# Kernel optimization log

Measured on AMD Instinct MI355X. Metric: run time of the kernel, lower is better.

The kernel has to match this reference:

```python
import jax, jax.numpy as jnp
import numpy as np

B, NS, NF, D, H = 64, 16, 4096, 128, 256  # batch, n_slots, n_feat, slot_dim, mlp_hidden
EPS_LN = 1e-5
EPS_ATT = 1e-8


def _layernorm(x, g, b):
    mu = x.mean(-1, keepdims=True)
    var = x.var(-1, keepdims=True)
    return (x - mu) / jnp.sqrt(var + EPS_LN) * g + b


def setup_inputs() -> dict:
    key = jax.random.key(0)
    ks = jax.random.split(key, 8)
    s = 0.02  # init scale for weights
    return {
        "t": jnp.zeros((), jnp.float32),
        "slots": jax.random.normal(ks[0], (B, NS, D), jnp.float32),
        "k": jax.random.normal(ks[1], (B, NF, D), jnp.float32),
        "v": jax.random.normal(ks[2], (B, NF, D), jnp.float32),
        "Wq": jax.random.normal(ks[3], (D, D), jnp.float32) * s,           # eqx Linear weight [out,in], no bias
        "ln_slots_g": jnp.ones((D,), jnp.float32),
        "ln_slots_b": jnp.zeros((D,), jnp.float32),
        "W_ih": jax.random.normal(ks[4], (3 * D, D), jnp.float32) * s,     # GRUCell input weights
        "W_hh": jax.random.normal(ks[5], (3 * D, D), jnp.float32) * s,     # GRUCell hidden weights
        "b_ih": jnp.zeros((3 * D,), jnp.float32),
        "b_n": jnp.zeros((D,), jnp.float32),
        "ln_ff_g": jnp.ones((D,), jnp.float32),
        "ln_ff_b": jnp.zeros((D,), jnp.float32),
        "W0": jax.random.normal(ks[6], (H, D), jnp.float32) * s,
        "b0": jnp.zeros((H,), jnp.float32),
        "W1": jax.random.normal(ks[7], (D, H), jnp.float32) * s,
        "b1": jnp.zeros((D,), jnp.float32),
    }


def reference(t, slots, k, v, Wq, ln_slots_g, ln_slots_b,
              W_ih, W_hh, b_ih, b_n, ln_ff_g, ln_ff_b, W0, b0, W1, b1):
    scale = D ** (-0.5)
    # LayerNorm over slot features, then query projection
    slots_norm = _layernorm(slots, ln_slots_g, ln_slots_b)
    q = jnp.einsum('bnd,ed->bne', slots_norm, Wq)                    # [B,NS,D]
    # Doubly-normalized slot attention: softmax over slots (axis=1), renorm over features
    att_logits = jnp.einsum('bnd,bmd->bnm', q, k) * scale            # [B,NS,NF]
    att = jax.nn.softmax(att_logits, axis=1)
    att = att / (att.sum(axis=-1, keepdims=True) + EPS_ATT)
    attended = jnp.einsum('bnm,bmd->bnd', att, v)                    # [B,NS,D]
    # GRUCell (equinox semantics): gates order (reset, input, new)
    igates = jnp.einsum('bnd,ed->bne', attended, W_ih) + b_ih        # [B,NS,3D]
    hgates = jnp.einsum('bnd,ed->bne', slots, W_hh)                  # [B,NS,3D]
    ir, ii, inew = jnp.split(igates, 3, axis=-1)
    hr, hi, hnew = jnp.split(hgates, 3, axis=-1)
    reset = jax.nn.sigmoid(ir + hr)
    inp = jax.nn.sigmoid(ii + hi)
    new = jnp.tanh(inew + reset * (hnew + b_n))
    gru_out = new + inp * (slots - new)                              # [B,NS,D]
    # LayerNorm -> MLP residual
    gru_normed = _layernorm(gru_out, ln_ff_g, ln_ff_b)
    h = jax.nn.relu(jnp.einsum('bnd,hd->bnh', gru_normed, W0) + b0)
    h = jnp.einsum('bnh,dh->bnd', h, W1) + b1
    target = gru_out + h
    return target - slots
```

## Files before the change

### kernel.cpp

```cpp
#include <hip/hip_runtime.h>
#include <hip/hip_bf16.h>
#include <math.h>

#define B_  64
#define NS_ 16
#define NF_ 4096
#define D_  128
#define H_  256


typedef __attribute__((ext_vector_type(8))) short bf16x8;
typedef __attribute__((ext_vector_type(4))) float f32x4;

__device__ __forceinline__ bf16x8 as_bf16x8(uint4 u) {
    union { uint4 u; bf16x8 h; } c; c.u = u; return c.h;
}

__device__ __forceinline__ unsigned int pk_bf16(float a, float b) {
    unsigned int ua = __float_as_uint(a), ub = __float_as_uint(b);
    ua = (ua + 0x7FFFu + ((ua >> 16) & 1u)) >> 16;
    ub = (ub + 0x7FFFu + ((ub >> 16) & 1u)) >> 16;
    return ua | (ub << 16);
}

__device__ __forceinline__ float dot4(float4 a, float4 b) {
    return a.x * b.x + a.y * b.y + a.z * b.z + a.w * b.w;
}

__global__ __launch_bounds__(128) void k_q(
    const float* __restrict__ slots, const float* __restrict__ Wq,
    const float* __restrict__ lng, const float* __restrict__ lnb,
    unsigned int* __restrict__ q_out, float* __restrict__ acc, float* __restrict__ den) {
    const int b = blockIdx.x;
    const int t = threadIdx.x;
    __shared__ float sl_s[16][128];
    __shared__ float norm_s[16][128];
    __shared__ float st_s[16][8][2];
    __shared__ float mu_s[16], rs_s[16];
    __shared__ float q_s[16][128];

    const float4* sp = (const float4*)(slots + (size_t)b * 2048);
#pragma unroll
    for (int i = 0; i < 4; ++i) {
        int f = i * 128 + t;
        *(float4*)&sl_s[f >> 5][(f & 31) * 4] = sp[f];
    }
    __syncthreads();

    {
        int n = t >> 3, j = t & 7;
        float s1 = 0.f, s2 = 0.f;
#pragma unroll
        for (int d2 = 0; d2 < 16; ++d2) {
            float x = sl_s[n][j * 16 + d2];
            s1 += x; s2 += x * x;
        }
        st_s[n][j][0] = s1; st_s[n][j][1] = s2;
    }
    __syncthreads();
    if (t < 16) {
        float s1 = 0.f, s2 = 0.f;
#pragma unroll
        for (int j = 0; j < 8; ++j) { s1 += st_s[t][j][0]; s2 += st_s[t][j][1]; }
        float mu = s1 * (1.0f / 128.0f);
        float var = s2 * (1.0f / 128.0f) - mu * mu;
        mu_s[t] = mu;
        rs_s[t] = rsqrtf(var + 1e-5f);
    }
    __syncthreads();

    float gl = lng[t], bl = lnb[t];
#pragma unroll
    for (int n = 0; n < 16; ++n)
        norm_s[n][t] = (sl_s[n][t] - mu_s[n]) * rs_s[n] * gl + bl;
    __syncthreads();

    const float4* wq = (const float4*)(Wq + (size_t)t * 128);
    float qn[16];
#pragma unroll
    for (int n = 0; n < 16; ++n) qn[n] = 0.f;
#pragma unroll 4
    for (int j = 0; j < 32; ++j) {
        float4 w4 = wq[j];
#pragma unroll
        for (int n = 0; n < 16; ++n) qn[n] += dot4(w4, *(const float4*)&norm_s[n][4 * j]);
    }
#pragma unroll
    for (int n = 0; n < 16; ++n) q_s[n][t] = qn[n];

    float4 z4 = make_float4(0.f, 0.f, 0.f, 0.f);
    float4* ab = (float4*)(acc + (size_t)b * 2048);
#pragma unroll
    for (int i = 0; i < 4; ++i) ab[i * 128 + t] = z4;
    if (t < 16) den[b * 16 + t] = 0.f;
    __syncthreads();

    unsigned int* qo = q_out + (size_t)b * 1024;
#pragma unroll
    for (int i = 0; i < 8; ++i) {
        int u = i * 128 + t;
        int n = u >> 6, e2 = u & 63;
        qo[n * 64 + e2] = pk_bf16(q_s[n][2 * e2], q_s[n][2 * e2 + 1]);
    }
}

__global__ __launch_bounds__(256) void k_attn(
    const float* __restrict__ kg_, const float* __restrict__ vg_,
    const unsigned int* __restrict__ q_u, float* __restrict__ acc_g, float* __restrict__ denom_g) {
    const int t = threadIdx.x;
    const int w = t >> 6, l = t & 63;
    const int b = blockIdx.y;
    const int lm = l & 15;
    const int g  = l >> 4;
    const int dcol = t & 127;
    const int nh = t >> 7;

    __shared__ unsigned int lds_u[5632];
    unsigned int* k_s = lds_u;
    float*        p_s = (float*)(lds_u + 4352);

    uint4 qA[4];
    {
        const uint4* qb = (const uint4*)q_u + ((b * 16 + lm) * 16);
#pragma unroll
        for (int kk = 0; kk < 4; ++kk) qA[kk] = qb[kk * 4 + g];
    }

    float acc[8];
#pragma unroll
    for (int i = 0; i < 8; ++i) acc[i] = 0.f;
    float dn[4] = {0.f, 0.f, 0.f, 0.f};

    const size_t mbase = (size_t)b * NF_ + blockIdx.x * 128;
    const float4* kg4 = (const float4*)kg_ + (mbase + w * 16) * 32;
    const float*  vgp = vg_ + mbase * 128 + dcol;

    for (int sub = 0; sub < 2; ++sub) {
        const float* vt = vgp + (size_t)sub * 64 * 128;

        float vva[8], vvb[8];
#pragma unroll
        for (int i = 0; i < 8; ++i) vva[i] = vt[i * 128];

        const float4* kp = kg4 + sub * 64 * 32;
#pragma unroll
        for (int c = 0; c < 4; ++c) {
            float4 t0 = kp[(2 * c) * 64 + l];
            float4 t1 = kp[(2 * c + 1) * 64 + l];
            int r0 = w * 16 + 2 * (2 * c) + (l >> 5);
            int r1 = w * 16 + 2 * (2 * c + 1) + (l >> 5);
            *(uint2*)&k_s[r0 * 68 + 2 * (l & 31)] =
                make_uint2(pk_bf16(t0.x, t0.y), pk_bf16(t0.z, t0.w));
            *(uint2*)&k_s[r1 * 68 + 2 * (l & 31)] =
                make_uint2(pk_bf16(t1.x, t1.y), pk_bf16(t1.z, t1.w));
        }

        f32x4 sacc = {0.f, 0.f, 0.f, 0.f};
#pragma unroll
        for (int kk = 0; kk < 4; ++kk) {
            uint4 kb = *(const uint4*)&k_s[(w * 16 + lm) * 68 + kk * 16 + g * 4];
            sacc = __builtin_amdgcn_mfma_f32_16x16x32_bf16(
                as_bf16x8(qA[kk]), as_bf16x8(kb), sacc, 0, 0, 0);
        }
        const float scale = 0.08838834764831845f;
        float e0 = __expf(sacc[0] * scale);
        float e1 = __expf(sacc[1] * scale);
        float e2 = __expf(sacc[2] * scale);
        float e3 = __expf(sacc[3] * scale);
        float se = (e0 + e1) + (e2 + e3);
        se += __shfl_xor(se, 16);
        se += __shfl_xor(se, 32);
        float rse = __builtin_amdgcn_rcpf(se);
        float4 pv4 = make_float4(e0 * rse, e1 * rse, e2 * rse, e3 * rse);
        dn[0] += pv4.x; dn[1] += pv4.y; dn[2] += pv4.z; dn[3] += pv4.w;
        *(float4*)&p_s[(w * 16 + lm) * 20 + g * 4] = pv4;
        __syncthreads();

#pragma unroll
        for (int op = 0; op < 4; ++op) {
            const int octA = 2 * op, octB = 2 * op + 1;
#pragma unroll
            for (int i = 0; i < 8; ++i) vvb[i] = vt[(octB * 8 + i) * 128];
#pragma unroll
            for (int i = 0; i < 8; ++i) {
                int m = octA * 8 + i;
                float4 pa = *(const float4*)&p_s[m * 20 + nh * 8];
                float4 pb = *(const float4*)&p_s[m * 20 + nh * 8 + 4];
                float vvi = vva[i];
                acc[0] = fmaf(pa.x, vvi, acc[0]);
                acc[1] = fmaf(pa.y, vvi, acc[1]);
                acc[2] = fmaf(pa.z, vvi, acc[2]);
                acc[3] = fmaf(pa.w, vvi, acc[3]);
                acc[4] = fmaf(pb.x, vvi, acc[4]);
                acc[5] = fmaf(pb.y, vvi, acc[5]);
                acc[6] = fmaf(pb.z, vvi, acc[6]);
                acc[7] = fmaf(pb.w, vvi, acc[7]);
            }
            if (op < 3) {
#pragma unroll
                for (int i = 0; i < 8; ++i) vva[i] = vt[((octB + 1) * 8 + i) * 128];
            }
#pragma unroll
            for (int i = 0; i < 8; ++i) {
                int m = octB * 8 + i;
                float4 pa = *(const float4*)&p_s[m * 20 + nh * 8];
                float4 pb = *(const float4*)&p_s[m * 20 + nh * 8 + 4];
                float vvi = vvb[i];
                acc[0] = fmaf(pa.x, vvi, acc[0]);
                acc[1] = fmaf(pa.y, vvi, acc[1]);
                acc[2] = fmaf(pa.z, vvi, acc[2]);
                acc[3] = fmaf(pa.w, vvi, acc[3]);
                acc[4] = fmaf(pb.x, vvi, acc[4]);
                acc[5] = fmaf(pb.y, vvi, acc[5]);
                acc[6] = fmaf(pb.z, vvi, acc[6]);
                acc[7] = fmaf(pb.w, vvi, acc[7]);
            }
        }
        __syncthreads();
    }

#pragma unroll
    for (int m = 1; m <= 8; m <<= 1) {
#pragma unroll
        for (int r = 0; r < 4; ++r) dn[r] += __shfl_xor(dn[r], m);
    }
    if (lm == 0) {
#pragma unroll
        for (int r = 0; r < 4; ++r)
            atomicAdd(denom_g + b * 16 + g * 4 + r, dn[r]);
    }
    float* base = acc_g + (size_t)b * 2048 + dcol;
#pragma unroll
    for (int i = 0; i < 8; ++i)
        atomicAdd(base + (nh * 8 + i) * 128, acc[i]);
}

__global__ __launch_bounds__(256) void k_final(
    const float* __restrict__ acc_g, const float* __restrict__ denom_g,
    const float* __restrict__ slots,
    const float* __restrict__ W_ih, const float* __restrict__ W_hh,
    const float* __restrict__ b_ih, const float* __restrict__ b_n,
    const float* __restrict__ ffg, const float* __restrict__ ffb,
    const float* __restrict__ W0, const float* __restrict__ b0,
    const float* __restrict__ W1, const float* __restrict__ b1,
    float* __restrict__ out) {
    const int bn0 = blockIdx.x * 4;
    const int t = threadIdx.x;
    __shared__ float att_s[4][128], slot_s[4][128];
    __shared__ float gates_s[4][4][128];
    __shared__ float gru_s[4][128], gn_s[4][128];
    __shared__ float h_s[4][256];

#pragma unroll
    for (int idx = t; idx < 512; idx += 256) {
        int bi = idx >> 7, d = idx & 127;
        int bn = bn0 + bi;
        float den = denom_g[bn] + 1e-8f;
        att_s[bi][d] = acc_g[(size_t)bn * 128 + d] / den;
        slot_s[bi][d] = slots[(size_t)bn * 128 + d];
    }
    __syncthreads();

    for (int g = t; g < 384; g += 256) {
        const float4* wi = (const float4*)(W_ih + (size_t)g * 128);
        const float4* wh = (const float4*)(W_hh + (size_t)g * 128);
        float si[4] = {0.f, 0.f, 0.f, 0.f}, sh[4] = {0.f, 0.f, 0.f, 0.f};
#pragma unroll 4
        for (int j = 0; j < 32; ++j) {
            float4 wi4 = wi[j], wh4 = wh[j];
#pragma unroll
            for (int bi = 0; bi < 4; ++bi) {
                si[bi] += dot4(wi4, *(const float4*)&att_s[bi][4 * j]);
                sh[bi] += dot4(wh4, *(const float4*)&slot_s[bi][4 * j]);
            }
        }
        float bih = b_ih[g];
        int d = g & 127;
#pragma unroll
        for (int bi = 0; bi < 4; ++bi) {
            if (g < 128)       gates_s[bi][0][d] = si[bi] + sh[bi] + bih;
            else if (g < 256)  gates_s[bi][1][d] = si[bi] + sh[bi] + bih;
            else { gates_s[bi][2][d] = si[bi] + bih; gates_s[bi][3][d] = sh[bi]; }
        }
    }
    __syncthreads();

    {
        int bi = t >> 6, l = t & 63;
        float gr[2], s1 = 0.f, s2 = 0.f;
#pragma unroll
        for (int h = 0; h < 2; ++h) {
            int d = l + 64 * h;
            float rr = 1.f / (1.f + __expf(-gates_s[bi][0][d]));
            float ii = 1.f / (1.f + __expf(-gates_s[bi][1][d]));
            float nv = tanhf(gates_s[bi][2][d] + rr * (gates_s[bi][3][d] + b_n[d]));
            float gru = nv + ii * (slot_s[bi][d] - nv);
            gr[h] = gru;
            gru_s[bi][d] = gru;
            s1 += gru; s2 += gru * gru;
        }
#pragma unroll
        for (int m = 1; m < 64; m <<= 1) { s1 += __shfl_xor(s1, m); s2 += __shfl_xor(s2, m); }
        float mu = s1 * (1.0f / 128.0f);
        float var = s2 * (1.0f / 128.0f) - mu * mu;
        float rstd = rsqrtf(var + 1e-5f);
#pragma unroll
        for (int h = 0; h < 2; ++h) {
            int d = l + 64 * h;
            gn_s[bi][d] = (gr[h] - mu) * rstd * ffg[d] + ffb[d];
        }
    }
    __syncthreads();

    {
        const float4* w0 = (const float4*)(W0 + (size_t)t * 128);
        float s[4] = {0.f, 0.f, 0.f, 0.f};
#pragma unroll 4
        for (int j = 0; j < 32; ++j) {
            float4 w4 = w0[j];
#pragma unroll
            for (int bi = 0; bi < 4; ++bi) s[bi] += dot4(w4, *(const float4*)&gn_s[bi][4 * j]);
        }
        float b0v = b0[t];
#pragma unroll
        for (int bi = 0; bi < 4; ++bi) h_s[bi][t] = fmaxf(s[bi] + b0v, 0.f);
    }
    __syncthreads();

    {
        int dr = t & 127, bp = (t >> 7) * 2;
        const float4* w1 = (const float4*)(W1 + (size_t)dr * 256);
        float s[2] = {0.f, 0.f};
#pragma unroll 4
        for (int j = 0; j < 64; ++j) {
            float4 w4 = w1[j];
#pragma unroll
            for (int u = 0; u < 2; ++u) s[u] += dot4(w4, *(const float4*)&h_s[bp + u][4 * j]);
        }
        float b1v = b1[dr];
#pragma unroll
        for (int u = 0; u < 2; ++u) {
            int bi = bp + u;
            out[(size_t)(bn0 + bi) * 128 + dr] = gru_s[bi][dr] + s[u] + b1v - slot_s[bi][dr];
        }
    }
}

extern "C" void kernel_launch(void* const* d_in, const int* in_sizes, int n_in,
                              void* d_out, int out_size, void* d_ws, size_t ws_size,
                              hipStream_t stream) {
    const float* slots = (const float*)d_in[1];
    const float* k     = (const float*)d_in[2];
    const float* v     = (const float*)d_in[3];
    const float* Wq    = (const float*)d_in[4];
    const float* lng   = (const float*)d_in[5];
    const float* lnb   = (const float*)d_in[6];
    const float* W_ih  = (const float*)d_in[7];
    const float* W_hh  = (const float*)d_in[8];
    const float* b_ih  = (const float*)d_in[9];
    const float* b_n   = (const float*)d_in[10];
    const float* ffg   = (const float*)d_in[11];
    const float* ffb   = (const float*)d_in[12];
    const float* W0    = (const float*)d_in[13];
    const float* b0    = (const float*)d_in[14];
    const float* W1    = (const float*)d_in[15];
    const float* b1    = (const float*)d_in[16];

    char* ws = (char*)d_ws;
    unsigned int* q_u = (unsigned int*)ws;
    float* acc = (float*)(ws + 262144);
    float* den = (float*)(ws + 786432);

    k_q<<<dim3(B_), dim3(128), 0, stream>>>(slots, Wq, lng, lnb, q_u, acc, den);
    k_attn<<<dim3(32, B_), dim3(256), 0, stream>>>(k, v, q_u, acc, den);
    k_final<<<dim3(256), dim3(256), 0, stream>>>(acc, den, slots, W_ih, W_hh,
                                                 b_ih, b_n, ffg, ffb, W0, b0, W1, b1,
                                                 (float*)d_out);
}
```

Measured before the change: 378.3 us.

## Split PV accumulation by feature rows and reduce halves in LDS before atomics

The P·V stage is repartitioned. Each thread half now covers 32 of the 64 feature rows for all 16 slots, instead of all 64 rows for 8 slots. The two halves' partial sums are combined through shared memory, so only half the threads issue global atomicAdds. The K tile and the first V rows are also loaded into registers up front so their latency overlaps the bf16 conversion. This raises accumulator register use, reuses the K LDS region for the reduction, and adds an extra barrier.

```diff
diff --git a/kernel.cpp b/kernel.cpp
--- a/kernel.cpp
+++ b/kernel.cpp
@@ -126,9 +126,9 @@
         for (int kk = 0; kk < 4; ++kk) qA[kk] = qb[kk * 4 + g];
     }
 
-    float acc[8];
-#pragma unroll
-    for (int i = 0; i < 8; ++i) acc[i] = 0.f;
+    float acc[16];
+#pragma unroll
+    for (int i = 0; i < 16; ++i) acc[i] = 0.f;
     float dn[4] = {0.f, 0.f, 0.f, 0.f};
 
     const size_t mbase = (size_t)b * NF_ + blockIdx.x * 128;
@@ -136,31 +136,40 @@
     const float*  vgp = vg_ + mbase * 128 + dcol;
 
     for (int sub = 0; sub < 2; ++sub) {
-        const float* vt = vgp + (size_t)sub * 64 * 128;
+        const float* vt = vgp + (size_t)(sub * 64 + nh * 32) * 128;
+
+        const float4* kp = kg4 + sub * 64 * 32;
+        float4 ka[4], kb4[4];
+#pragma unroll
+        for (int i = 0; i < 4; ++i) ka[i] = kp[i * 64 + l];
+#pragma unroll
+        for (int i = 0; i < 4; ++i) kb4[i] = kp[(4 + i) * 64 + l];
 
         float vva[8], vvb[8];
 #pragma unroll
         for (int i = 0; i < 8; ++i) vva[i] = vt[i * 128];
-
-        const float4* kp = kg4 + sub * 64 * 32;
-#pragma unroll
-        for (int c = 0; c < 4; ++c) {
-            float4 t0 = kp[(2 * c) * 64 + l];
-            float4 t1 = kp[(2 * c + 1) * 64 + l];
-            int r0 = w * 16 + 2 * (2 * c) + (l >> 5);
-            int r1 = w * 16 + 2 * (2 * c + 1) + (l >> 5);
-            *(uint2*)&k_s[r0 * 68 + 2 * (l & 31)] =
-                make_uint2(pk_bf16(t0.x, t0.y), pk_bf16(t0.z, t0.w));
-            *(uint2*)&k_s[r1 * 68 + 2 * (l & 31)] =
-                make_uint2(pk_bf16(t1.x, t1.y), pk_bf16(t1.z, t1.w));
+#pragma unroll
+        for (int i = 0; i < 8; ++i) vvb[i] = vt[(8 + i) * 128];
+
+#pragma unroll
+        for (int i = 0; i < 4; ++i) {
+            int r = w * 16 + 2 * i + (l >> 5);
+            *(uint2*)&k_s[r * 68 + 2 * (l & 31)] =
+                make_uint2(pk_bf16(ka[i].x, ka[i].y), pk_bf16(ka[i].z, ka[i].w));
+        }
+#pragma unroll
+        for (int i = 0; i < 4; ++i) {
+            int r = w * 16 + 2 * (4 + i) + (l >> 5);
+            *(uint2*)&k_s[r * 68 + 2 * (l & 31)] =
+                make_uint2(pk_bf16(kb4[i].x, kb4[i].y), pk_bf16(kb4[i].z, kb4[i].w));
         }
 
         f32x4 sacc = {0.f, 0.f, 0.f, 0.f};
 #pragma unroll
         for (int kk = 0; kk < 4; ++kk) {
-            uint4 kb = *(const uint4*)&k_s[(w * 16 + lm) * 68 + kk * 16 + g * 4];
+            uint4 kf = *(const uint4*)&k_s[(w * 16 + lm) * 68 + kk * 16 + g * 4];
             sacc = __builtin_amdgcn_mfma_f32_16x16x32_bf16(
-                as_bf16x8(qA[kk]), as_bf16x8(kb), sacc, 0, 0, 0);
+                as_bf16x8(qA[kk]), as_bf16x8(kf), sacc, 0, 0, 0);
         }
         const float scale = 0.08838834764831845f;
         float e0 = __expf(sacc[0] * scale);
@@ -176,46 +185,43 @@
         *(float4*)&p_s[(w * 16 + lm) * 20 + g * 4] = pv4;
         __syncthreads();
 
-#pragma unroll
-        for (int op = 0; op < 4; ++op) {
-            const int octA = 2 * op, octB = 2 * op + 1;
-#pragma unroll
-            for (int i = 0; i < 8; ++i) vvb[i] = vt[(octB * 8 + i) * 128];
-#pragma unroll
-            for (int i = 0; i < 8; ++i) {
-                int m = octA * 8 + i;
-                float4 pa = *(const float4*)&p_s[m * 20 + nh * 8];
-                float4 pb = *(const float4*)&p_s[m * 20 + nh * 8 + 4];
-                float vvi = vva[i];
-                acc[0] = fmaf(pa.x, vvi, acc[0]);
-                acc[1] = fmaf(pa.y, vvi, acc[1]);
-                acc[2] = fmaf(pa.z, vvi, acc[2]);
-                acc[3] = fmaf(pa.w, vvi, acc[3]);
-                acc[4] = fmaf(pb.x, vvi, acc[4]);
-                acc[5] = fmaf(pb.y, vvi, acc[5]);
-                acc[6] = fmaf(pb.z, vvi, acc[6]);
-                acc[7] = fmaf(pb.w, vvi, acc[7]);
-            }
-            if (op < 3) {
-#pragma unroll
-                for (int i = 0; i < 8; ++i) vva[i] = vt[((octB + 1) * 8 + i) * 128];
-            }
-#pragma unroll
-            for (int i = 0; i < 8; ++i) {
-                int m = octB * 8 + i;
-                float4 pa = *(const float4*)&p_s[m * 20 + nh * 8];
-                float4 pb = *(const float4*)&p_s[m * 20 + nh * 8 + 4];
-                float vvi = vvb[i];
-                acc[0] = fmaf(pa.x, vvi, acc[0]);
-                acc[1] = fmaf(pa.y, vvi, acc[1]);
-                acc[2] = fmaf(pa.z, vvi, acc[2]);
-                acc[3] = fmaf(pa.w, vvi, acc[3]);
-                acc[4] = fmaf(pb.x, vvi, acc[4]);
-                acc[5] = fmaf(pb.y, vvi, acc[5]);
-                acc[6] = fmaf(pb.z, vvi, acc[6]);
-                acc[7] = fmaf(pb.w, vvi, acc[7]);
-            }
-        }
+#define PV_CONSUME(VREG, BASE)                                              \
+        {                                                                   \
+            _Pragma("unroll")                                               \
+            for (int i = 0; i < 8; ++i) {                                   \
+                int m = nh * 32 + (BASE) + i;                               \
+                float vvi = VREG[i];                                        \
+                float4 pa = *(const float4*)&p_s[m * 20 + 0];               \
+                float4 pb = *(const float4*)&p_s[m * 20 + 4];               \
+                float4 pc = *(const float4*)&p_s[m * 20 + 8];               \
+                float4 pd = *(const float4*)&p_s[m * 20 + 12];              \
+                acc[0]  = fmaf(pa.x, vvi, acc[0]);                          \
+                acc[1]  = fmaf(pa.y, vvi, acc[1]);                          \
+                acc[2]  = fmaf(pa.z, vvi, acc[2]);                          \
+                acc[3]  = fmaf(pa.w, vvi, acc[3]);                          \
+                acc[4]  = fmaf(pb.x, vvi, acc[4]);                          \
+                acc[5]  = fmaf(pb.y, vvi, acc[5]);                          \
+                acc[6]  = fmaf(pb.z, vvi, acc[6]);                          \
+                acc[7]  = fmaf(pb.w, vvi, acc[7]);                          \
+                acc[8]  = fmaf(pc.x, vvi, acc[8]);                          \
+                acc[9]  = fmaf(pc.y, vvi, acc[9]);                          \
+                acc[10] = fmaf(pc.z, vvi, acc[10]);                         \
+                acc[11] = fmaf(pc.w, vvi, acc[11]);                         \
+                acc[12] = fmaf(pd.x, vvi, acc[12]);                         \
+                acc[13] = fmaf(pd.y, vvi, acc[13]);                         \
+                acc[14] = fmaf(pd.z, vvi, acc[14]);                         \
+                acc[15] = fmaf(pd.w, vvi, acc[15]);                         \
+            }                                                               \
+        }
+        PV_CONSUME(vva, 0)
+#pragma unroll
+        for (int i = 0; i < 8; ++i) vva[i] = vt[(16 + i) * 128];
+        PV_CONSUME(vvb, 8)
+#pragma unroll
+        for (int i = 0; i < 8; ++i) vvb[i] = vt[(24 + i) * 128];
+        PV_CONSUME(vva, 16)
+        PV_CONSUME(vvb, 24)
+#undef PV_CONSUME
         __syncthreads();
     }
 
@@ -229,10 +235,19 @@
         for (int r = 0; r < 4; ++r)
             atomicAdd(denom_g + b * 16 + g * 4 + r, dn[r]);
     }
-    float* base = acc_g + (size_t)b * 2048 + dcol;
-#pragma unroll
-    for (int i = 0; i < 8; ++i)
-        atomicAdd(base + (nh * 8 + i) * 128, acc[i]);
+    float* red = (float*)lds_u;
+    if (nh == 1) {
+#pragma unroll
+        for (int i = 0; i < 4; ++i)
+            *(float4*)&red[dcol * 16 + 4 * i] = *(const float4*)&acc[4 * i];
+    }
+    __syncthreads();
+    if (nh == 0) {
+        float* base = acc_g + (size_t)b * 2048 + dcol;
+#pragma unroll
+        for (int n = 0; n < 16; ++n)
+            atomicAdd(base + n * 128, acc[n] + red[dcol * 16 + n]);
+    }
 }
 
 __global__ __launch_bounds__(256) void k_final(
```

Measured after the change: 375.8 us. No clear change (-0.7%).

## Stage V via direct global-to-LDS loads, feed K straight to MFMA registers

Applied to the files above, without the earlier changes.

K rows are now loaded directly into registers in the MFMA operand layout and converted to bf16 there, dropping the K LDS staging buffer. The V tile is copied into LDS with global_load_lds, asynchronous to the QK MFMA and softmax. The PV product is re-split so each half-block covers 32 features for all 16 slots. The two halves are then combined in LDS before the atomics, which halves the global atomic count. This costs more LDS (about 37KB per block) and an extra barrier, and may lower occupancy.

```diff
diff --git a/kernel.cpp b/kernel.cpp
--- a/kernel.cpp
+++ b/kernel.cpp
@@ -115,9 +115,9 @@
     const int dcol = t & 127;
     const int nh = t >> 7;
 
-    __shared__ unsigned int lds_u[5632];
-    unsigned int* k_s = lds_u;
-    float*        p_s = (float*)(lds_u + 4352);
+    __shared__ unsigned int lds_u[9472];
+    float* v_l = (float*)lds_u;
+    float* p_s = (float*)(lds_u + 8192);
 
     uint4 qA[4];
     {
@@ -126,42 +126,43 @@
         for (int kk = 0; kk < 4; ++kk) qA[kk] = qb[kk * 4 + g];
     }
 
-    float acc[8];
-#pragma unroll
-    for (int i = 0; i < 8; ++i) acc[i] = 0.f;
+    float acc[16];
+#pragma unroll
+    for (int i = 0; i < 16; ++i) acc[i] = 0.f;
     float dn[4] = {0.f, 0.f, 0.f, 0.f};
 
     const size_t mbase = (size_t)b * NF_ + blockIdx.x * 128;
-    const float4* kg4 = (const float4*)kg_ + (mbase + w * 16) * 32;
-    const float*  vgp = vg_ + mbase * 128 + dcol;
 
     for (int sub = 0; sub < 2; ++sub) {
-        const float* vt = vgp + (size_t)sub * 64 * 128;
-
-        float vva[8], vvb[8];
-#pragma unroll
-        for (int i = 0; i < 8; ++i) vva[i] = vt[i * 128];
-
-        const float4* kp = kg4 + sub * 64 * 32;
-#pragma unroll
-        for (int c = 0; c < 4; ++c) {
-            float4 t0 = kp[(2 * c) * 64 + l];
-            float4 t1 = kp[(2 * c + 1) * 64 + l];
-            int r0 = w * 16 + 2 * (2 * c) + (l >> 5);
-            int r1 = w * 16 + 2 * (2 * c + 1) + (l >> 5);
-            *(uint2*)&k_s[r0 * 68 + 2 * (l & 31)] =
-                make_uint2(pk_bf16(t0.x, t0.y), pk_bf16(t0.z, t0.w));
-            *(uint2*)&k_s[r1 * 68 + 2 * (l & 31)] =
-                make_uint2(pk_bf16(t1.x, t1.y), pk_bf16(t1.z, t1.w));
-        }
+        const float* krow = kg_ + (mbase + sub * 64 + w * 16 + lm) * 128 + g * 8;
+        float4 ka[4], kb2[4];
+#pragma unroll
+        for (int kk = 0; kk < 4; ++kk) {
+            ka[kk]  = *(const float4*)(krow + kk * 32);
+            kb2[kk] = *(const float4*)(krow + kk * 32 + 4);
+        }
+
+        const float* vsub = vg_ + (mbase + sub * 64) * 128;
+#pragma unroll
+        for (int i = 0; i < 8; ++i) {
+            const int chunk = w * 8 + i;
+            __builtin_amdgcn_global_load_lds(
+                (const unsigned int*)(vsub + chunk * 256 + l * 4),
+                (unsigned int*)(v_l + chunk * 256), 16, 0, 0);
+        }
+
+        uint4 kf[4];
+#pragma unroll
+        for (int kk = 0; kk < 4; ++kk)
+            kf[kk] = make_uint4(pk_bf16(ka[kk].x, ka[kk].y), pk_bf16(ka[kk].z, ka[kk].w),
+                                pk_bf16(kb2[kk].x, kb2[kk].y), pk_bf16(kb2[kk].z, kb2[kk].w));
 
         f32x4 sacc = {0.f, 0.f, 0.f, 0.f};
 #pragma unroll
-        for (int kk = 0; kk < 4; ++kk) {
-            uint4 kb = *(const uint4*)&k_s[(w * 16 + lm) * 68 + kk * 16 + g * 4];
+        for (int kk = 0; kk < 4; ++kk)
             sacc = __builtin_amdgcn_mfma_f32_16x16x32_bf16(
-                as_bf16x8(qA[kk]), as_bf16x8(kb), sacc, 0, 0, 0);
-        }
+                as_bf16x8(qA[kk]), as_bf16x8(kf[kk]), sacc, 0, 0, 0);
+
         const float scale = 0.08838834764831845f;
         float e0 = __expf(sacc[0] * scale);
         float e1 = __expf(sacc[1] * scale);
@@ -174,47 +175,33 @@
         float4 pv4 = make_float4(e0 * rse, e1 * rse, e2 * rse, e3 * rse);
         dn[0] += pv4.x; dn[1] += pv4.y; dn[2] += pv4.z; dn[3] += pv4.w;
         *(float4*)&p_s[(w * 16 + lm) * 20 + g * 4] = pv4;
+
         __syncthreads();
 
-#pragma unroll
-        for (int op = 0; op < 4; ++op) {
-            const int octA = 2 * op, octB = 2 * op + 1;
-#pragma unroll
-            for (int i = 0; i < 8; ++i) vvb[i] = vt[(octB * 8 + i) * 128];
-#pragma unroll
-            for (int i = 0; i < 8; ++i) {
-                int m = octA * 8 + i;
-                float4 pa = *(const float4*)&p_s[m * 20 + nh * 8];
-                float4 pb = *(const float4*)&p_s[m * 20 + nh * 8 + 4];
-                float vvi = vva[i];
-                acc[0] = fmaf(pa.x, vvi, acc[0]);
-                acc[1] = fmaf(pa.y, vvi, acc[1]);
-                acc[2] = fmaf(pa.z, vvi, acc[2]);
-                acc[3] = fmaf(pa.w, vvi, acc[3]);
-                acc[4] = fmaf(pb.x, vvi, acc[4]);
-                acc[5] = fmaf(pb.y, vvi, acc[5]);
-                acc[6] = fmaf(pb.z, vvi, acc[6]);
-                acc[7] = fmaf(pb.w, vvi, acc[7]);
-            }
-            if (op < 3) {
-#pragma unroll
-                for (int i = 0; i < 8; ++i) vva[i] = vt[((octB + 1) * 8 + i) * 128];
-            }
-#pragma unroll
-            for (int i = 0; i < 8; ++i) {
-                int m = octB * 8 + i;
-                float4 pa = *(const float4*)&p_s[m * 20 + nh * 8];
-                float4 pb = *(const float4*)&p_s[m * 20 + nh * 8 + 4];
-                float vvi = vvb[i];
-                acc[0] = fmaf(pa.x, vvi, acc[0]);
-                acc[1] = fmaf(pa.y, vvi, acc[1]);
-                acc[2] = fmaf(pa.z, vvi, acc[2]);
-                acc[3] = fmaf(pa.w, vvi, acc[3]);
-                acc[4] = fmaf(pb.x, vvi, acc[4]);
-                acc[5] = fmaf(pb.y, vvi, acc[5]);
-                acc[6] = fmaf(pb.z, vvi, acc[6]);
-                acc[7] = fmaf(pb.w, vvi, acc[7]);
-            }
+#pragma unroll 8
+        for (int i = 0; i < 32; ++i) {
+            int m = nh * 32 + i;
+            float vvi = v_l[m * 128 + dcol];
+            float4 pa = *(const float4*)&p_s[m * 20 + 0];
+            float4 pb = *(const float4*)&p_s[m * 20 + 4];
+            float4 pc = *(const float4*)&p_s[m * 20 + 8];
+            float4 pd = *(const float4*)&p_s[m * 20 + 12];
+            acc[0]  = fmaf(pa.x, vvi, acc[0]);
+            acc[1]  = fmaf(pa.y, vvi, acc[1]);
+            acc[2]  = fmaf(pa.z, vvi, acc[2]);
+            acc[3]  = fmaf(pa.w, vvi, acc[3]);
+            acc[4]  = fmaf(pb.x, vvi, acc[4]);
+            acc[5]  = fmaf(pb.y, vvi, acc[5]);
+            acc[6]  = fmaf(pb.z, vvi, acc[6]);
+            acc[7]  = fmaf(pb.w, vvi, acc[7]);
+            acc[8]  = fmaf(pc.x, vvi, acc[8]);
+            acc[9]  = fmaf(pc.y, vvi, acc[9]);
+            acc[10] = fmaf(pc.z, vvi, acc[10]);
+            acc[11] = fmaf(pc.w, vvi, acc[11]);
+            acc[12] = fmaf(pd.x, vvi, acc[12]);
+            acc[13] = fmaf(pd.y, vvi, acc[13]);
+            acc[14] = fmaf(pd.z, vvi, acc[14]);
+            acc[15] = fmaf(pd.w, vvi, acc[15]);
         }
         __syncthreads();
     }
@@ -229,10 +216,18 @@
         for (int r = 0; r < 4; ++r)
             atomicAdd(denom_g + b * 16 + g * 4 + r, dn[r]);
     }
-    float* base = acc_g + (size_t)b * 2048 + dcol;
-#pragma unroll
-    for (int i = 0; i < 8; ++i)
-        atomicAdd(base + (nh * 8 + i) * 128, acc[i]);
+    float* red = (float*)lds_u;
+    if (nh == 1) {
+#pragma unroll
+        for (int n = 0; n < 16; ++n) red[dcol * 17 + n] = acc[n];
+    }
+    __syncthreads();
+    if (nh == 0) {
+        float* base = acc_g + (size_t)b * 2048 + dcol;
+#pragma unroll
+        for (int n = 0; n < 16; ++n)
+            atomicAdd(base + n * 128, acc[n] + red[dcol * 17 + n]);
+    }
 }
 
 __global__ __launch_bounds__(256) void k_final(
```

Result: no change. 378.9 us (+0.2%).
